# Kernel tuning notes

Hardware: AMD Instinct MI355X
Metric: run time of the kernel (lower is better)

## Reference

```python
import jax, jax.numpy as jnp
import numpy as np

B, L, H = 16, 32, 768
E, R, T = 200000, 512, 2000000
NUM_STEPS = 2
EPS = 1e-6


def setup_inputs() -> dict:
    key = jax.random.key(0)
    ks = jax.random.split(key, 16)
    s = 1.0 / np.sqrt(H)
    return {
        'heads': jax.random.uniform(ks[0], (B, E), jnp.float32),
        'q_word_h': jax.random.normal(ks[1], (B, L, H), jnp.float32),
        'attention_mask': jnp.ones((B, L), jnp.float32),
        'subj': jax.random.randint(ks[2], (T,), 0, E),
        'rel': jax.random.randint(ks[3], (T,), 0, R),
        'obj': jax.random.randint(ks[4], (T,), 0, E),
        'key_w': jax.random.normal(ks[5], (H, H), jnp.float32) * s,
        'key_b': jnp.zeros((H,), jnp.float32),
        'rel_w': jax.random.normal(ks[6], (H, R), jnp.float32) * s,
        'rel_b': jnp.zeros((R,), jnp.float32),
        'hop_w': jax.random.normal(ks[7], (H, 1), jnp.float32) * s,
        'hop_b': jnp.zeros((1,), jnp.float32),
        'hw_w': jax.random.normal(ks[8], (H, H), jnp.float32) * s,
        'hw_b': jnp.zeros((H,), jnp.float32),
    }


def _follow(e, r, subj, rel, obj, num_ent):
    # x[b,t] = e[b, subj[t]] * r[b, rel[t]]  (== Msubj@e.T * Mrel@r.T)
    x = e[:, subj] * r[:, rel]                      # [B, T]
    # scatter-add over object entities (== Mobj.T @ x)
    return jnp.zeros((e.shape[0], num_ent), e.dtype).at[:, obj].add(x)


def reference(heads, q_word_h, attention_mask, subj, rel, obj,
              key_w, key_b, rel_w, rel_b, hop_w, hop_b, hw_w, hw_b):
    mask = attention_mask[:, None, :]               # [B,1,L]
    last_e = heads
    q_hop = q_word_h
    prev_ctx = None                                  # q_word_h_dist_ctx[-1]
    ent_probs, ctx_h_list = [], []
    for t in range(NUM_STEPS):
        h_key = q_hop @ key_w + key_b                # [B,L,H]
        # torch: (h_key @ q_word_h^T)^T -> logits[b,i,j] = q_word_h[b,i].h_key[b,j]
        q_logits = jnp.einsum('bih,bjh->bij', q_word_h, h_key)
        q_dist = jax.nn.softmax(q_logits, axis=2) * mask
        q_dist = q_dist / (jnp.sum(q_dist, axis=2, keepdims=True) + EPS)
        hop_ctx = jnp.einsum('bij,bjh->bih', q_dist, q_hop)
        if t == 0:
            q_hop = q_word_h + hop_ctx
            prev_ctx = hop_ctx
        else:
            z = jax.nn.sigmoid(prev_ctx @ hw_w + hw_b)
            q_hop = q_word_h + hop_ctx + z * prev_ctx
            prev_ctx = hop_ctx + z * prev_ctx
        q_word_att = jax.nn.softmax(jnp.sum(q_dist, axis=1, keepdims=True), axis=2) * mask
        q_word_att = q_word_att / (jnp.sum(q_word_att, axis=2, keepdims=True) + EPS)  # [B,1,L]
        ctx_h = jnp.einsum('blh,bl->bh', q_hop, q_word_att[:, 0, :])
        ctx_h_list.append(ctx_h)
        rel_dist = jax.nn.sigmoid(ctx_h @ rel_w + rel_b)   # [B,R]
        new_e = _follow(last_e, rel_dist, subj, rel, obj, heads.shape[1])
        # clamp-by-division with detached scale
        z_norm = jax.lax.stop_gradient(jnp.where(new_e > 1.0, new_e, 1.0))
        last_e = new_e / z_norm
        ent_probs.append(last_e)
    hop_res = jnp.stack(ent_probs, axis=1)           # [B,S,E]
    ctx_hist = jnp.stack(ctx_h_list, axis=1)         # [B,S,H]
    hop_logit = ctx_hist @ hop_w + hop_b             # [B,S,1]
    hop_attn = jax.nn.softmax(hop_logit, axis=1)     # softmax over hops
    e_score = jnp.sum(hop_res * hop_attn, axis=1)    # [B,E]
    return e_score
```

## Files before the change

### kernel.cpp

```cpp
#include <hip/hip_runtime.h>
#include <hip/hip_bf16.h>
#include <math.h>

#define NB 16
#define NL 32
#define NH 768
#define NE 200000
#define NR 512
#define NT 2000000
#define FEPS 1e-6f

typedef float f32x4 __attribute__((ext_vector_type(4)));

__global__ __launch_bounds__(256) void k_transpose(const float* __restrict__ heads,
                                                   float* __restrict__ headsT) {
  __shared__ float tile[256][17];
  int e0 = blockIdx.x * 256;
  int tid = threadIdx.x;
  if (e0 + tid < NE) {
#pragma unroll
    for (int b = 0; b < NB; ++b)
      tile[tid][b] = heads[(size_t)b * NE + e0 + tid];
  }
  __syncthreads();
#pragma unroll
  for (int j = 0; j < 16; ++j) {
    int idx = j * 256 + tid;
    int i = idx >> 4, b = idx & 15;
    if (e0 + i < NE) headsT[(size_t)(e0 + i) * NB + b] = tile[i][b];
  }
}

__global__ __launch_bounds__(256) void k_rowmm2(const float* __restrict__ X0,
                                                const float* __restrict__ W0,
                                                const float* __restrict__ b0,
                                                float* __restrict__ Y0, int act0,
                                                const float* __restrict__ X1,
                                                const float* __restrict__ W1,
                                                const float* __restrict__ b1,
                                                float* __restrict__ Y1, int act1,
                                                int nblk0) {
  const float* X; const float* W; const float* bias; float* Y; int act, row0;
  int blk = blockIdx.x;
  if (blk < nblk0) { X = X0; W = W0; bias = b0; Y = Y0; act = act0; row0 = blk * 2; }
  else            { X = X1; W = W1; bias = b1; Y = Y1; act = act1; row0 = (blk - nblk0) * 2; }

  __shared__ float xs[2][NH];
  int tid = threadIdx.x;
  for (int r = 0; r < 2; ++r)
    for (int k = tid; k < NH; k += 256)
      xs[r][k] = X[(size_t)(row0 + r) * NH + k];
  __syncthreads();

  float acc[2][3] = {};
  for (int k = 0; k < NH; ++k) {
    float w0 = W[(size_t)k * NH + tid];
    float w1 = W[(size_t)k * NH + tid + 256];
    float w2 = W[(size_t)k * NH + tid + 512];
#pragma unroll
    for (int r = 0; r < 2; ++r) {
      float x = xs[r][k];
      acc[r][0] = fmaf(x, w0, acc[r][0]);
      acc[r][1] = fmaf(x, w1, acc[r][1]);
      acc[r][2] = fmaf(x, w2, acc[r][2]);
    }
  }
  float bb0 = bias[tid], bb1 = bias[tid + 256], bb2 = bias[tid + 512];
#pragma unroll
  for (int r = 0; r < 2; ++r) {
    size_t base = (size_t)(row0 + r) * NH;
    float y0 = acc[r][0] + bb0, y1 = acc[r][1] + bb1, y2 = acc[r][2] + bb2;
    if (act == 1) {
      y0 = 1.f / (1.f + expf(-y0));
      y1 = 1.f / (1.f + expf(-y1));
      y2 = 1.f / (1.f + expf(-y2));
    }
    Y[base + tid] = y0;
    Y[base + tid + 256] = y1;
    Y[base + tid + 512] = y2;
  }
}

__global__ __launch_bounds__(1024) void k_attn(const float* __restrict__ qwh,
                                               const float* __restrict__ hkey,
                                               const float* __restrict__ mask,
                                               float* __restrict__ q_dist,
                                               float* __restrict__ att) {
  int b = blockIdx.x;
  int tid = threadIdx.x;
  int i = tid >> 5, j = tid & 31;
  __shared__ float hks[32 * 129];
  __shared__ float qs[32 * 129];
  __shared__ float qd[32 * 33];

  float acc = 0.f;
  for (int k0 = 0; k0 < NH; k0 += 128) {
    __syncthreads();
    {
      int jj = tid >> 5;
      int kk4 = tid & 31;
      size_t goff = ((size_t)b * NL + jj) * NH + k0 + kk4 * 4;
      f32x4 hv = *(const f32x4*)(hkey + goff);
      f32x4 qv = *(const f32x4*)(qwh + goff);
      int base = jj * 129 + kk4 * 4;
      hks[base] = hv.x; hks[base + 1] = hv.y; hks[base + 2] = hv.z; hks[base + 3] = hv.w;
      qs[base] = qv.x;  qs[base + 1] = qv.y;  qs[base + 2] = qv.z;  qs[base + 3] = qv.w;
    }
    __syncthreads();
#pragma unroll 8
    for (int kk = 0; kk < 128; ++kk)
      acc = fmaf(qs[i * 129 + kk], hks[j * 129 + kk], acc);
  }

  float m = acc;
  for (int s = 16; s; s >>= 1) m = fmaxf(m, __shfl_xor(m, s, 32));
  float ex = expf(acc - m);
  float sum = ex;
  for (int s = 16; s; s >>= 1) sum += __shfl_xor(sum, s, 32);
  float p = ex / sum;
  p *= mask[b * NL + j];
  float s2 = p;
  for (int s = 16; s; s >>= 1) s2 += __shfl_xor(s2, s, 32);
  p = p / (s2 + FEPS);

  q_dist[((size_t)b * NL + i) * NL + j] = p;
  qd[i * 33 + j] = p;
  __syncthreads();

  if (tid < 32) {
    int jj = tid;
    float c = 0.f;
    for (int ii = 0; ii < 32; ++ii) c += qd[ii * 33 + jj];
    float mm = c;
    for (int s = 16; s; s >>= 1) mm = fmaxf(mm, __shfl_xor(mm, s, 32));
    float e2 = expf(c - mm);
    float ss = e2;
    for (int s = 16; s; s >>= 1) ss += __shfl_xor(ss, s, 32);
    float a = e2 / ss;
    a *= mask[b * NL + jj];
    float s3 = a;
    for (int s = 16; s; s >>= 1) s3 += __shfl_xor(s3, s, 32);
    a = a / (s3 + FEPS);
    att[b * NL + jj] = a;
  }
}

template <int STEP>
__global__ __launch_bounds__(256) void k_update_rel(const float* __restrict__ qwh,
                                                    const float* __restrict__ qhop_old,
                                                    const float* __restrict__ q_dist,
                                                    const float* __restrict__ att,
                                                    const float* __restrict__ zbuf,
                                                    const float* __restrict__ pc_old,
                                                    float* __restrict__ qhop_new,
                                                    float* __restrict__ pc_new,
                                                    float* __restrict__ ctx_h,
                                                    const float* __restrict__ rel_w,
                                                    const float* __restrict__ rel_b,
                                                    float* __restrict__ relT) {
  int b = blockIdx.x;
  int tid = threadIdx.x;
  __shared__ float qd[NL * NL];
  __shared__ float as[NL];
  __shared__ float ctx_s[NH];
  for (int idx = tid; idx < NL * NL; idx += 256) qd[idx] = q_dist[(size_t)b * NL * NL + idx];
  if (tid < NL) as[tid] = att[b * NL + tid];
  __syncthreads();

  float qh0[NL], qh1[NL], qh2[NL];
#pragma unroll
  for (int j = 0; j < NL; ++j) {
    const float* p = qhop_old + ((size_t)b * NL + j) * NH + tid;
    qh0[j] = p[0];
    qh1[j] = p[256];
    qh2[j] = p[512];
  }

  float c0 = 0.f, c1 = 0.f, c2 = 0.f;
  for (int l = 0; l < NL; ++l) {
    float h0 = 0.f, h1 = 0.f, h2 = 0.f;
#pragma unroll
    for (int j = 0; j < NL; ++j) {
      float d = qd[l * NL + j];
      h0 = fmaf(d, qh0[j], h0);
      h1 = fmaf(d, qh1[j], h1);
      h2 = fmaf(d, qh2[j], h2);
    }
    size_t base = ((size_t)b * NL + l) * NH + tid;
    float qn0, qn1, qn2;
    if (STEP == 0) {
      qn0 = qwh[base] + h0;
      qn1 = qwh[base + 256] + h1;
      qn2 = qwh[base + 512] + h2;
      qhop_new[base] = qn0;
      qhop_new[base + 256] = qn1;
      qhop_new[base + 512] = qn2;
      pc_new[base] = h0;
      pc_new[base + 256] = h1;
      pc_new[base + 512] = h2;
    } else {
      float t0 = zbuf[base] * pc_old[base];
      float t1 = zbuf[base + 256] * pc_old[base + 256];
      float t2 = zbuf[base + 512] * pc_old[base + 512];
      qn0 = qwh[base] + h0 + t0;
      qn1 = qwh[base + 256] + h1 + t1;
      qn2 = qwh[base + 512] + h2 + t2;
    }
    float a = as[l];
    c0 = fmaf(a, qn0, c0);
    c1 = fmaf(a, qn1, c1);
    c2 = fmaf(a, qn2, c2);
  }
  size_t cb = ((size_t)b * 2 + STEP) * NH + tid;
  ctx_h[cb] = c0;
  ctx_h[cb + 256] = c1;
  ctx_h[cb + 512] = c2;
  ctx_s[tid] = c0;
  ctx_s[tid + 256] = c1;
  ctx_s[tid + 512] = c2;
  __syncthreads();

  float accA = rel_b[tid], accB = rel_b[tid + 256];
  for (int h = 0; h < NH; ++h) {
    float c = ctx_s[h];
    accA = fmaf(c, rel_w[(size_t)h * NR + tid], accA);
    accB = fmaf(c, rel_w[(size_t)h * NR + tid + 256], accB);
  }
  relT[tid * NB + b] = 1.f / (1.f + expf(-accA));
  relT[(tid + 256) * NB + b] = 1.f / (1.f + expf(-accB));
}

template <int CLAMP>
__global__ __launch_bounds__(256) void k_follow(const int* __restrict__ subj,
                                                const int* __restrict__ rel,
                                                const int* __restrict__ obj,
                                                const float* __restrict__ srcT,
                                                const float* __restrict__ relT,
                                                float* __restrict__ dstT) {
  const size_t stride = (size_t)gridDim.x * 256;
  size_t gid = (size_t)blockIdx.x * 256 + threadIdx.x;
#pragma unroll 4
  for (int it = 0; it < 4; ++it, gid += stride) {
    int k = (int)(gid >> 4);
    int b = (int)(gid & 15);
    int s = __builtin_nontemporal_load(&subj[k]);
    int r = __builtin_nontemporal_load(&rel[k]);
    int o = __builtin_nontemporal_load(&obj[k]);
    float x = srcT[(size_t)s * NB + b];
    if (CLAMP) x = fminf(x, 1.f);
    x *= relT[r * NB + b];
    atomicAdd(&dstT[(size_t)o * NB + b], x);
  }
}

__global__ __launch_bounds__(256) void k_combine(const float* __restrict__ e0T,
                                                 const float* __restrict__ e1T,
                                                 const float* __restrict__ ctx_h,
                                                 const float* __restrict__ hop_w,
                                                 const float* __restrict__ hop_b,
                                                 float* __restrict__ out) {
  __shared__ float s0[256 * 17], s1[256 * 17];
  __shared__ float lg[32];
  __shared__ float ha[32];
  int tid = threadIdx.x;

  {
    int pair = tid >> 3, sub = tid & 7;
    int bb = pair >> 1, t = pair & 1;
    float acc = 0.f;
    for (int h = sub; h < NH; h += 8)
      acc = fmaf(ctx_h[((size_t)bb * 2 + t) * NH + h], hop_w[h], acc);
    for (int s = 4; s; s >>= 1) acc += __shfl_xor(acc, s, 8);
    if (sub == 0) lg[pair] = acc + hop_b[0];
  }
  __syncthreads();
  if (tid < 16) {
    float l0 = lg[tid * 2], l1 = lg[tid * 2 + 1];
    float m = fmaxf(l0, l1);
    float e0 = expf(l0 - m), e1 = expf(l1 - m);
    float s = e0 + e1;
    ha[tid * 2] = e0 / s;
    ha[tid * 2 + 1] = e1 / s;
  }
  __syncthreads();

  int e0 = blockIdx.x * 256;
#pragma unroll
  for (int j = 0; j < 16; ++j) {
    int idx = j * 256 + tid;
    int i = idx >> 4, b = idx & 15;
    if (e0 + i < NE) {
      s0[i * 17 + b] = fminf(e0T[(size_t)e0 * NB + idx], 1.f);
      s1[i * 17 + b] = fminf(e1T[(size_t)e0 * NB + idx], 1.f);
    }
  }
  __syncthreads();
  if (e0 + tid < NE) {
#pragma unroll
    for (int b = 0; b < NB; ++b) {
      float a0 = ha[b * 2], a1 = ha[b * 2 + 1];
      out[(size_t)b * NE + e0 + tid] = a0 * s0[tid * 17 + b] + a1 * s1[tid * 17 + b];
    }
  }
}

extern "C" void kernel_launch(void* const* d_in, const int* in_sizes, int n_in,
                              void* d_out, int out_size, void* d_ws, size_t ws_size,
                              hipStream_t stream) {
  const float* heads = (const float*)d_in[0];
  const float* q_word_h = (const float*)d_in[1];
  const float* mask = (const float*)d_in[2];
  const int* subj = (const int*)d_in[3];
  const int* rel = (const int*)d_in[4];
  const int* obj = (const int*)d_in[5];
  const float* key_w = (const float*)d_in[6];
  const float* key_b = (const float*)d_in[7];
  const float* rel_w = (const float*)d_in[8];
  const float* rel_b = (const float*)d_in[9];
  const float* hop_w = (const float*)d_in[10];
  const float* hop_b = (const float*)d_in[11];
  const float* hw_w = (const float*)d_in[12];
  const float* hw_b = (const float*)d_in[13];

  float* ws = (float*)d_ws;
  size_t o = 0;
  float* headsT = ws + o; o += (size_t)NE * NB;
  float* e0T    = ws + o; o += (size_t)NE * NB;
  float* e1T    = ws + o; o += (size_t)NE * NB;
  float* h_key  = ws + o; o += (size_t)NB * NL * NH;
  float* qhopB  = ws + o; o += (size_t)NB * NL * NH;
  float* pcB    = ws + o; o += (size_t)NB * NL * NH;
  float* zbuf   = ws + o; o += (size_t)NB * NL * NH;
  float* q_dist = ws + o; o += (size_t)NB * NL * NL;
  float* att    = ws + o; o += (size_t)NB * NL;
  float* ctx_h  = ws + o; o += (size_t)NB * 2 * NH;
  float* relT   = ws + o; o += (size_t)NR * NB;

  const int EB_BLOCKS = (NE + 255) / 256;
  const int FOLLOW_BLOCKS = (NT * 16) / (256 * 4);
  const int MM_BLOCKS = (NB * NL) / 2;

  hipMemsetAsync(e0T, 0, (size_t)2 * NE * NB * sizeof(float), stream);
  k_transpose<<<EB_BLOCKS, 256, 0, stream>>>(heads, headsT);

  k_rowmm2<<<MM_BLOCKS, 256, 0, stream>>>(q_word_h, key_w, key_b, h_key, 0,
                                          q_word_h, key_w, key_b, h_key, 0, MM_BLOCKS);
  k_attn<<<NB, 1024, 0, stream>>>(q_word_h, h_key, mask, q_dist, att);
  k_update_rel<0><<<NB, 256, 0, stream>>>(q_word_h, q_word_h, q_dist, att, nullptr,
                                          nullptr, qhopB, pcB, ctx_h, rel_w, rel_b, relT);
  k_follow<0><<<FOLLOW_BLOCKS, 256, 0, stream>>>(subj, rel, obj, headsT, relT, e0T);

  k_rowmm2<<<2 * MM_BLOCKS, 256, 0, stream>>>(qhopB, key_w, key_b, h_key, 0,
                                              pcB, hw_w, hw_b, zbuf, 1, MM_BLOCKS);
  k_attn<<<NB, 1024, 0, stream>>>(q_word_h, h_key, mask, q_dist, att);
  k_update_rel<1><<<NB, 256, 0, stream>>>(q_word_h, qhopB, q_dist, att, zbuf, pcB,
                                          nullptr, nullptr, ctx_h, rel_w, rel_b, relT);
  k_follow<1><<<FOLLOW_BLOCKS, 256, 0, stream>>>(subj, rel, obj, e0T, relT, e1T);

  k_combine<<<EB_BLOCKS, 256, 0, stream>>>(e0T, e1T, ctx_h, hop_w, hop_b, (float*)d_out);
}
```

Measured before the change: 592.3 us.

## Build CSR by object and replace atomic scatter follow with gather

Each call now builds a CSR index of triples grouped by object entity, using a histogram, a three-stage prefix scan and an atomic fill. The two follow steps then become per-entity gathers with no float atomics, and the zeroing memset of the output buffers is dropped. The goal is to remove the cost of 32M float atomic adds per step. In exchange the CSR build adds several kernels and 2M integer atomics per call, and the gather has load imbalance across entities. The path only runs if the workspace is large enough, otherwise the old scatter path is used.

Result: slower. 735.9 us (+24.2%).

```diff
diff --git a/kernel.cpp b/kernel.cpp
--- a/kernel.cpp
+++ b/kernel.cpp
@@ -9,6 +9,9 @@
 #define NR 512
 #define NT 2000000
 #define FEPS 1e-6f
+
+#define EB_BLOCKS ((NE + 255) / 256)
+#define NT_BLOCKS ((NT + 255) / 256)
 
 typedef float f32x4 __attribute__((ext_vector_type(4)));
 
@@ -230,6 +233,97 @@
   relT[(tid + 256) * NB + b] = 1.f / (1.f + expf(-accB));
 }
 
+__global__ __launch_bounds__(256) void k_hist(const int* __restrict__ obj,
+                                              int* __restrict__ deg) {
+  int k = blockIdx.x * 256 + threadIdx.x;
+  if (k < NT) atomicAdd(&deg[obj[k]], 1);
+}
+
+__global__ __launch_bounds__(256) void k_scan1(const int* __restrict__ deg,
+                                               int* __restrict__ bsum) {
+  int e = blockIdx.x * 256 + threadIdx.x;
+  int v = (e < NE) ? deg[e] : 0;
+#pragma unroll
+  for (int s = 32; s; s >>= 1) v += __shfl_down(v, s, 64);
+  __shared__ int wsum[4];
+  if ((threadIdx.x & 63) == 0) wsum[threadIdx.x >> 6] = v;
+  __syncthreads();
+  if (threadIdx.x == 0) bsum[blockIdx.x] = wsum[0] + wsum[1] + wsum[2] + wsum[3];
+}
+
+__global__ __launch_bounds__(1024) void k_scan2(const int* __restrict__ bsum,
+                                                int* __restrict__ bbase,
+                                                int* __restrict__ off) {
+  __shared__ int s[1024];
+  int t = threadIdx.x;
+  int v = (t < EB_BLOCKS) ? bsum[t] : 0;
+  s[t] = v;
+  __syncthreads();
+  for (int d = 1; d < 1024; d <<= 1) {
+    int x = (t >= d) ? s[t - d] : 0;
+    __syncthreads();
+    s[t] += x;
+    __syncthreads();
+  }
+  if (t < EB_BLOCKS) bbase[t] = s[t] - v;
+  if (t == 0) off[NE] = NT;
+}
+
+__global__ __launch_bounds__(256) void k_scan3(const int* __restrict__ deg,
+                                               const int* __restrict__ bbase,
+                                               int* __restrict__ off,
+                                               int* __restrict__ cursor) {
+  __shared__ int s[256];
+  int t = threadIdx.x;
+  int e = blockIdx.x * 256 + t;
+  int v = (e < NE) ? deg[e] : 0;
+  s[t] = v;
+  __syncthreads();
+  for (int d = 1; d < 256; d <<= 1) {
+    int x = (t >= d) ? s[t - d] : 0;
+    __syncthreads();
+    s[t] += x;
+    __syncthreads();
+  }
+  if (e < NE) {
+    int o = bbase[blockIdx.x] + s[t] - v;
+    off[e] = o;
+    cursor[e] = o;
+  }
+}
+
+__global__ __launch_bounds__(256) void k_fill(const int* __restrict__ subj,
+                                              const int* __restrict__ rel,
+                                              const int* __restrict__ obj,
+                                              int* __restrict__ cursor,
+                                              int2* __restrict__ csr) {
+  int k = blockIdx.x * 256 + threadIdx.x;
+  if (k < NT) {
+    int o = obj[k];
+    int pos = atomicAdd(&cursor[o], 1);
+    csr[pos] = make_int2(subj[k], rel[k]);
+  }
+}
+
+template <int CLAMP>
+__global__ __launch_bounds__(256) void k_follow_csr(const int* __restrict__ off,
+                                                    const int2* __restrict__ csr,
+                                                    const float* __restrict__ srcT,
+                                                    const float* __restrict__ relT,
+                                                    float* __restrict__ dstT) {
+  int e = blockIdx.x * 16 + (threadIdx.x >> 4);
+  int b = threadIdx.x & 15;
+  int i0 = off[e], i1 = off[e + 1];
+  float acc = 0.f;
+  for (int idx = i0; idx < i1; ++idx) {
+    int2 sr = csr[idx];
+    float x = srcT[(size_t)sr.x * NB + b];
+    if (CLAMP) x = fminf(x, 1.f);
+    acc = fmaf(x, relT[sr.y * NB + b], acc);
+  }
+  dstT[(size_t)e * NB + b] = acc;
+}
+
 template <int CLAMP>
 __global__ __launch_bounds__(256) void k_follow(const int* __restrict__ subj,
                                                 const int* __restrict__ rel,
@@ -335,12 +429,31 @@
   float* att    = ws + o; o += (size_t)NB * NL;
   float* ctx_h  = ws + o; o += (size_t)NB * 2 * NH;
   float* relT   = ws + o; o += (size_t)NR * NB;
-
-  const int EB_BLOCKS = (NE + 255) / 256;
+  o = (o + 1) & ~(size_t)1;
+  int* deg    = (int*)(ws + o); o += NE;
+  int* off    = (int*)(ws + o); o += NE + 1;
+  int* cursor = (int*)(ws + o); o += NE;
+  int* bsum   = (int*)(ws + o); o += EB_BLOCKS;
+  int* bbase  = (int*)(ws + o); o += EB_BLOCKS;
+  o = (o + 1) & ~(size_t)1;
+  int2* csr   = (int2*)(ws + o); o += (size_t)NT * 2;
+
+  const bool use_csr = ws_size >= o * sizeof(float);
+
+  const int MM_BLOCKS = (NB * NL) / 2;
   const int FOLLOW_BLOCKS = (NT * 16) / (256 * 4);
-  const int MM_BLOCKS = (NB * NL) / 2;
-
-  hipMemsetAsync(e0T, 0, (size_t)2 * NE * NB * sizeof(float), stream);
+  const int CSR_FOLLOW_BLOCKS = NE / 16;
+
+  if (use_csr) {
+    hipMemsetAsync(deg, 0, (size_t)NE * sizeof(int), stream);
+    k_hist<<<NT_BLOCKS, 256, 0, stream>>>(obj, deg);
+    k_scan1<<<EB_BLOCKS, 256, 0, stream>>>(deg, bsum);
+    k_scan2<<<1, 1024, 0, stream>>>(bsum, bbase, off);
+    k_scan3<<<EB_BLOCKS, 256, 0, stream>>>(deg, bbase, off, cursor);
+    k_fill<<<NT_BLOCKS, 256, 0, stream>>>(subj, rel, obj, cursor, csr);
+  } else {
+    hipMemsetAsync(e0T, 0, (size_t)2 * NE * NB * sizeof(float), stream);
+  }
   k_transpose<<<EB_BLOCKS, 256, 0, stream>>>(heads, headsT);
 
   k_rowmm2<<<MM_BLOCKS, 256, 0, stream>>>(q_word_h, key_w, key_b, h_key, 0,
@@ -348,14 +461,20 @@
   k_attn<<<NB, 1024, 0, stream>>>(q_word_h, h_key, mask, q_dist, att);
   k_update_rel<0><<<NB, 256, 0, stream>>>(q_word_h, q_word_h, q_dist, att, nullptr,
                                           nullptr, qhopB, pcB, ctx_h, rel_w, rel_b, relT);
-  k_follow<0><<<FOLLOW_BLOCKS, 256, 0, stream>>>(subj, rel, obj, headsT, relT, e0T);
+  if (use_csr)
+    k_follow_csr<0><<<CSR_FOLLOW_BLOCKS, 256, 0, stream>>>(off, csr, headsT, relT, e0T);
+  else
+    k_follow<0><<<FOLLOW_BLOCKS, 256, 0, stream>>>(subj, rel, obj, headsT, relT, e0T);
 
   k_rowmm2<<<2 * MM_BLOCKS, 256, 0, stream>>>(qhopB, key_w, key_b, h_key, 0,
                                               pcB, hw_w, hw_b, zbuf, 1, MM_BLOCKS);
   k_attn<<<NB, 1024, 0, stream>>>(q_word_h, h_key, mask, q_dist, att);
   k_update_rel<1><<<NB, 256, 0, stream>>>(q_word_h, qhopB, q_dist, att, zbuf, pcB,
                                           nullptr, nullptr, ctx_h, rel_w, rel_b, relT);
-  k_follow<1><<<FOLLOW_BLOCKS, 256, 0, stream>>>(subj, rel, obj, e0T, relT, e1T);
+  if (use_csr)
+    k_follow_csr<1><<<CSR_FOLLOW_BLOCKS, 256, 0, stream>>>(off, csr, e0T, relT, e1T);
+  else
+    k_follow<1><<<FOLLOW_BLOCKS, 256, 0, stream>>>(subj, rel, obj, e0T, relT, e1T);
 
   k_combine<<<EB_BLOCKS, 256, 0, stream>>>(e0T, e1T, ctx_h, hop_w, hop_b, (float*)d_out);
 }
```

## Fuse attention with hop update and fold buffer zeroing into transpose

Applied to the files above, without the earlier changes.

Merges the attention kernel and the hop-update/relation kernel into one per-batch 1024-thread kernel. The full q_word_h slice is staged in shared memory and q_dist/att stay on chip instead of going through global buffers. The memset of the entity buffers is also folded into the transpose kernel, which cuts two launches per step plus one memset. The trade-off is a large shared-memory footprint (about 120KB) and only 16 blocks doing the serial rel_w matvec with 512 threads.

New measurement: 559.9 us. 1.06x faster.

```diff
diff --git a/kernel.cpp b/kernel.cpp
--- a/kernel.cpp
+++ b/kernel.cpp
@@ -10,10 +10,14 @@
 #define NT 2000000
 #define FEPS 1e-6f
 
+#define EB_BLOCKS ((NE + 255) / 256)
+
 typedef float f32x4 __attribute__((ext_vector_type(4)));
 
-__global__ __launch_bounds__(256) void k_transpose(const float* __restrict__ heads,
-                                                   float* __restrict__ headsT) {
+__global__ __launch_bounds__(256) void k_transpose_zero(const float* __restrict__ heads,
+                                                        float* __restrict__ headsT,
+                                                        float* __restrict__ e0T,
+                                                        float* __restrict__ e1T) {
   __shared__ float tile[256][17];
   int e0 = blockIdx.x * 256;
   int tid = threadIdx.x;
@@ -21,6 +25,18 @@
 #pragma unroll
     for (int b = 0; b < NB; ++b)
       tile[tid][b] = heads[(size_t)b * NE + e0 + tid];
+  }
+  {
+    f32x4 z = {0.f, 0.f, 0.f, 0.f};
+#pragma unroll
+    for (int j = 0; j < 4; ++j) {
+      int idx4 = j * 256 + tid;
+      size_t base = (size_t)e0 * NB + idx4 * 4;
+      if (base < (size_t)NE * NB) {
+        *(f32x4*)(e0T + base) = z;
+        *(f32x4*)(e1T + base) = z;
+      }
+    }
   }
   __syncthreads();
 #pragma unroll
@@ -81,35 +97,50 @@
   }
 }
 
-__global__ __launch_bounds__(1024) void k_attn(const float* __restrict__ qwh,
-                                               const float* __restrict__ hkey,
-                                               const float* __restrict__ mask,
-                                               float* __restrict__ q_dist,
-                                               float* __restrict__ att) {
+template <int STEP>
+__global__ __launch_bounds__(1024) void k_attn_update(const float* __restrict__ qwh,
+                                                      const float* __restrict__ hkey,
+                                                      const float* __restrict__ mask,
+                                                      const float* __restrict__ qhop_old,
+                                                      const float* __restrict__ zbuf,
+                                                      const float* __restrict__ pc_old,
+                                                      float* __restrict__ qhop_new,
+                                                      float* __restrict__ pc_new,
+                                                      float* __restrict__ ctx_h,
+                                                      const float* __restrict__ rel_w,
+                                                      const float* __restrict__ rel_b,
+                                                      float* __restrict__ relT) {
   int b = blockIdx.x;
   int tid = threadIdx.x;
+  __shared__ float qs_full[NL * NH];
+  __shared__ float hks[32 * 129];
+  __shared__ float qd[32 * 33];
+  __shared__ float ctx_s[NH];
+  __shared__ float as[NL];
+
+#pragma unroll
+  for (int it = 0; it < 6; ++it) {
+    int idx4 = it * 1024 + tid;
+    f32x4 v = *(const f32x4*)(qwh + (size_t)b * NL * NH + idx4 * 4);
+    *(f32x4*)(qs_full + idx4 * 4) = v;
+  }
+  __syncthreads();
+
   int i = tid >> 5, j = tid & 31;
-  __shared__ float hks[32 * 129];
-  __shared__ float qs[32 * 129];
-  __shared__ float qd[32 * 33];
-
   float acc = 0.f;
   for (int k0 = 0; k0 < NH; k0 += 128) {
-    __syncthreads();
     {
       int jj = tid >> 5;
       int kk4 = tid & 31;
-      size_t goff = ((size_t)b * NL + jj) * NH + k0 + kk4 * 4;
-      f32x4 hv = *(const f32x4*)(hkey + goff);
-      f32x4 qv = *(const f32x4*)(qwh + goff);
+      f32x4 hv = *(const f32x4*)(hkey + ((size_t)b * NL + jj) * NH + k0 + kk4 * 4);
       int base = jj * 129 + kk4 * 4;
       hks[base] = hv.x; hks[base + 1] = hv.y; hks[base + 2] = hv.z; hks[base + 3] = hv.w;
-      qs[base] = qv.x;  qs[base + 1] = qv.y;  qs[base + 2] = qv.z;  qs[base + 3] = qv.w;
     }
     __syncthreads();
 #pragma unroll 8
     for (int kk = 0; kk < 128; ++kk)
-      acc = fmaf(qs[i * 129 + kk], hks[j * 129 + kk], acc);
+      acc = fmaf(qs_full[i * NH + k0 + kk], hks[j * 129 + kk], acc);
+    __syncthreads();
   }
 
   float m = acc;
@@ -122,8 +153,6 @@
   float s2 = p;
   for (int s = 16; s; s >>= 1) s2 += __shfl_xor(s2, s, 32);
   p = p / (s2 + FEPS);
-
-  q_dist[((size_t)b * NL + i) * NL + j] = p;
   qd[i * 33 + j] = p;
   __syncthreads();
 
@@ -140,94 +169,50 @@
     a *= mask[b * NL + jj];
     float s3 = a;
     for (int s = 16; s; s >>= 1) s3 += __shfl_xor(s3, s, 32);
-    a = a / (s3 + FEPS);
-    att[b * NL + jj] = a;
-  }
-}
-
-template <int STEP>
-__global__ __launch_bounds__(256) void k_update_rel(const float* __restrict__ qwh,
-                                                    const float* __restrict__ qhop_old,
-                                                    const float* __restrict__ q_dist,
-                                                    const float* __restrict__ att,
-                                                    const float* __restrict__ zbuf,
-                                                    const float* __restrict__ pc_old,
-                                                    float* __restrict__ qhop_new,
-                                                    float* __restrict__ pc_new,
-                                                    float* __restrict__ ctx_h,
-                                                    const float* __restrict__ rel_w,
-                                                    const float* __restrict__ rel_b,
-                                                    float* __restrict__ relT) {
-  int b = blockIdx.x;
-  int tid = threadIdx.x;
-  __shared__ float qd[NL * NL];
-  __shared__ float as[NL];
-  __shared__ float ctx_s[NH];
-  for (int idx = tid; idx < NL * NL; idx += 256) qd[idx] = q_dist[(size_t)b * NL * NL + idx];
-  if (tid < NL) as[tid] = att[b * NL + tid];
-  __syncthreads();
-
-  float qh0[NL], qh1[NL], qh2[NL];
-#pragma unroll
-  for (int j = 0; j < NL; ++j) {
-    const float* p = qhop_old + ((size_t)b * NL + j) * NH + tid;
-    qh0[j] = p[0];
-    qh1[j] = p[256];
-    qh2[j] = p[512];
-  }
-
-  float c0 = 0.f, c1 = 0.f, c2 = 0.f;
-  for (int l = 0; l < NL; ++l) {
-    float h0 = 0.f, h1 = 0.f, h2 = 0.f;
-#pragma unroll
-    for (int j = 0; j < NL; ++j) {
-      float d = qd[l * NL + j];
-      h0 = fmaf(d, qh0[j], h0);
-      h1 = fmaf(d, qh1[j], h1);
-      h2 = fmaf(d, qh2[j], h2);
-    }
-    size_t base = ((size_t)b * NL + l) * NH + tid;
-    float qn0, qn1, qn2;
-    if (STEP == 0) {
-      qn0 = qwh[base] + h0;
-      qn1 = qwh[base + 256] + h1;
-      qn2 = qwh[base + 512] + h2;
-      qhop_new[base] = qn0;
-      qhop_new[base + 256] = qn1;
-      qhop_new[base + 512] = qn2;
-      pc_new[base] = h0;
-      pc_new[base + 256] = h1;
-      pc_new[base + 512] = h2;
-    } else {
-      float t0 = zbuf[base] * pc_old[base];
-      float t1 = zbuf[base + 256] * pc_old[base + 256];
-      float t2 = zbuf[base + 512] * pc_old[base + 512];
-      qn0 = qwh[base] + h0 + t0;
-      qn1 = qwh[base + 256] + h1 + t1;
-      qn2 = qwh[base + 512] + h2 + t2;
-    }
-    float a = as[l];
-    c0 = fmaf(a, qn0, c0);
-    c1 = fmaf(a, qn1, c1);
-    c2 = fmaf(a, qn2, c2);
-  }
-  size_t cb = ((size_t)b * 2 + STEP) * NH + tid;
-  ctx_h[cb] = c0;
-  ctx_h[cb + 256] = c1;
-  ctx_h[cb + 512] = c2;
-  ctx_s[tid] = c0;
-  ctx_s[tid + 256] = c1;
-  ctx_s[tid + 512] = c2;
-  __syncthreads();
-
-  float accA = rel_b[tid], accB = rel_b[tid + 256];
-  for (int h = 0; h < NH; ++h) {
-    float c = ctx_s[h];
-    accA = fmaf(c, rel_w[(size_t)h * NR + tid], accA);
-    accB = fmaf(c, rel_w[(size_t)h * NR + tid + 256], accB);
-  }
-  relT[tid * NB + b] = 1.f / (1.f + expf(-accA));
-  relT[(tid + 256) * NB + b] = 1.f / (1.f + expf(-accB));
+    as[jj] = a / (s3 + FEPS);
+  }
+  __syncthreads();
+
+  if (tid < NH) {
+    int h = tid;
+    float qh[NL];
+#pragma unroll
+    for (int jj = 0; jj < NL; ++jj) {
+      if (STEP == 0)
+        qh[jj] = qs_full[jj * NH + h];
+      else
+        qh[jj] = qhop_old[((size_t)b * NL + jj) * NH + h];
+    }
+    float c = 0.f;
+    for (int l = 0; l < NL; ++l) {
+      float hop = 0.f;
+#pragma unroll
+      for (int jj = 0; jj < NL; ++jj)
+        hop = fmaf(qd[l * 33 + jj], qh[jj], hop);
+      size_t base = ((size_t)b * NL + l) * NH + h;
+      float qn;
+      if (STEP == 0) {
+        qn = qs_full[l * NH + h] + hop;
+        qhop_new[base] = qn;
+        pc_new[base] = hop;
+      } else {
+        float t = zbuf[base] * pc_old[base];
+        qn = qs_full[l * NH + h] + hop + t;
+      }
+      c = fmaf(as[l], qn, c);
+    }
+    ctx_h[((size_t)b * 2 + STEP) * NH + h] = c;
+    ctx_s[h] = c;
+  }
+  __syncthreads();
+
+  if (tid < NR) {
+    int r = tid;
+    float a = rel_b[r];
+    for (int h = 0; h < NH; ++h)
+      a = fmaf(ctx_s[h], rel_w[(size_t)h * NR + r], a);
+    relT[r * NB + b] = 1.f / (1.f + expf(-a));
+  }
 }
 
 template <int CLAMP>
@@ -331,30 +316,26 @@
   float* qhopB  = ws + o; o += (size_t)NB * NL * NH;
   float* pcB    = ws + o; o += (size_t)NB * NL * NH;
   float* zbuf   = ws + o; o += (size_t)NB * NL * NH;
-  float* q_dist = ws + o; o += (size_t)NB * NL * NL;
-  float* att    = ws + o; o += (size_t)NB * NL;
   float* ctx_h  = ws + o; o += (size_t)NB * 2 * NH;
   float* relT   = ws + o; o += (size_t)NR * NB;
 
-  const int EB_BLOCKS = (NE + 255) / 256;
+  const int MM_BLOCKS = (NB * NL) / 2;
   const int FOLLOW_BLOCKS = (NT * 16) / (256 * 4);
-  const int MM_BLOCKS = (NB * NL) / 2;
-
-  hipMemsetAsync(e0T, 0, (size_t)2 * NE * NB * sizeof(float), stream);
-  k_transpose<<<EB_BLOCKS, 256, 0, stream>>>(heads, headsT);
+
+  k_transpose_zero<<<EB_BLOCKS, 256, 0, stream>>>(heads, headsT, e0T, e1T);
 
   k_rowmm2<<<MM_BLOCKS, 256, 0, stream>>>(q_word_h, key_w, key_b, h_key, 0,
                                           q_word_h, key_w, key_b, h_key, 0, MM_BLOCKS);
-  k_attn<<<NB, 1024, 0, stream>>>(q_word_h, h_key, mask, q_dist, att);
-  k_update_rel<0><<<NB, 256, 0, stream>>>(q_word_h, q_word_h, q_dist, att, nullptr,
-                                          nullptr, qhopB, pcB, ctx_h, rel_w, rel_b, relT);
+  k_attn_update<0><<<NB, 1024, 0, stream>>>(q_word_h, h_key, mask, q_word_h,
+                                            nullptr, nullptr, qhopB, pcB, ctx_h,
+                                            rel_w, rel_b, relT);
   k_follow<0><<<FOLLOW_BLOCKS, 256, 0, stream>>>(subj, rel, obj, headsT, relT, e0T);
 
   k_rowmm2<<<2 * MM_BLOCKS, 256, 0, stream>>>(qhopB, key_w, key_b, h_key, 0,
                                               pcB, hw_w, hw_b, zbuf, 1, MM_BLOCKS);
-  k_attn<<<NB, 1024, 0, stream>>>(q_word_h, h_key, mask, q_dist, att);
-  k_update_rel<1><<<NB, 256, 0, stream>>>(q_word_h, qhopB, q_dist, att, zbuf, pcB,
-                                          nullptr, nullptr, ctx_h, rel_w, rel_b, relT);
+  k_attn_update<1><<<NB, 1024, 0, stream>>>(q_word_h, h_key, mask, qhopB,
+                                            zbuf, pcB, nullptr, nullptr, ctx_h,
+                                            rel_w, rel_b, relT);
   k_follow<1><<<FOLLOW_BLOCKS, 256, 0, stream>>>(subj, rel, obj, e0T, relT, e1T);
 
   k_combine<<<EB_BLOCKS, 256, 0, stream>>>(e0T, e1T, ctx_h, hop_w, hop_b, (float*)d_out);
```
